# Kernel tuning notes

Hardware: AMD Instinct MI355X
Metric: run time of the kernel (lower is better)

## Reference

```python
import jax, jax.numpy as jnp
import numpy as np

WINDOW_SIZE = 11
SIGMA = 1.5
C1 = 0.01 ** 2
C2 = 0.03 ** 2


def _make_window(window_size, channel):
    x = np.arange(window_size) - window_size // 2
    g = np.exp(-(x ** 2) / (2.0 * SIGMA ** 2))
    g = g / g.sum()
    w2d = np.outer(g, g).astype(np.float32)  # [K,K]
    # depthwise kernel [C, 1, K, K]
    return jnp.asarray(np.broadcast_to(w2d, (channel, 1, window_size, window_size)).copy())


def _dw_conv(x, window, channel):
    pad = WINDOW_SIZE // 2
    return jax.lax.conv_general_dilated(
        x, window, window_strides=(1, 1), padding=[(pad, pad), (pad, pad)],
        dimension_numbers=('NCHW', 'OIHW', 'NCHW'), feature_group_count=channel)


def setup_inputs() -> dict:
    key = jax.random.key(0)
    k1, k2 = jax.random.split(key)
    shape = (16, 3, 512, 512)
    img1 = jax.random.uniform(k1, shape, dtype=jnp.float32)
    img2 = jax.random.uniform(k2, shape, dtype=jnp.float32)
    return {"img1": img1, "img2": img2}


def reference(img1, img2):
    channel = img1.shape[1]
    window = _make_window(WINDOW_SIZE, channel).astype(img1.dtype)

    mu1 = _dw_conv(img1, window, channel)
    mu2 = _dw_conv(img2, window, channel)
    mu1_sq = mu1 * mu1
    mu2_sq = mu2 * mu2
    mu1_mu2 = mu1 * mu2

    sigma1_sq = _dw_conv(img1 * img1, window, channel) - mu1_sq
    sigma2_sq = _dw_conv(img2 * img2, window, channel) - mu2_sq
    sigma12 = _dw_conv(img1 * img2, window, channel) - mu1_mu2

    ssim_map = ((2 * mu1_mu2 + C1) * (2 * sigma12 + C2)) / (
        (mu1_sq + mu2_sq + C1) * (sigma1_sq + sigma2_sq + C2))
    return jnp.mean(ssim_map)  # size_average=True
```

## Files before the change

kernel.cpp:

```cpp
#include <hip/hip_runtime.h>
#include <math.h>

#define IMG_H 512
#define IMG_W 512
#define TH 8
#define KR 5
#define KS 11
#define NR (TH + 2 * KR)
#define LWE 524
#define NTHREADS 512
#define NBANDS (IMG_H / TH)
#define NPLANES 48
#define NBLK (NBANDS * NPLANES)

typedef float f32x2 __attribute__((ext_vector_type(2)));
typedef float f32x4 __attribute__((ext_vector_type(4)));

struct W22 { float w[2 * KS]; };

__device__ __forceinline__ int swz(int e) { return e ^ ((e >> 3) & 7); }

__global__ __launch_bounds__(NTHREADS, 4)
void ssim_tile_kernel(const float* __restrict__ img1, const float* __restrict__ img2,
                      float* __restrict__ bsums, W22 wt) {
    __shared__ f32x4 sE[TH][LWE];
    __shared__ float redw[NTHREADS / 64];

    const int bid   = blockIdx.x;
    const int sbid  = (bid & 7) * (NBLK / 8) + (bid >> 3);
    const int plane = sbid >> 6;
    const int band  = sbid & (NBANDS - 1);

    const int r0 = band * TH - KR;
    const float* __restrict__ p1 = img1 + (size_t)plane * (IMG_H * IMG_W);
    const float* __restrict__ p2 = img2 + (size_t)plane * (IMG_H * IMG_W);
    const int tid = threadIdx.x;

    if (tid < 128) {
        const int h = tid & 15;
        if (h < 12) {
            const int r = tid >> 4;
            const int e = (h < 6) ? h : (512 + h);
            sE[r][swz(e)] = (f32x4){0.f, 0.f, 0.f, 0.f};
        }
    }

    float av[NR], bv[NR];
    {
        const float* __restrict__ g1 = p1 + tid;
        const float* __restrict__ g2 = p2 + tid;
        if (r0 >= 0 && r0 + NR <= IMG_H) {
            #pragma unroll
            for (int j = 0; j < NR; ++j) {
                av[j] = g1[(r0 + j) * IMG_W];
                bv[j] = g2[(r0 + j) * IMG_W];
            }
        } else {
            #pragma unroll
            for (int j = 0; j < NR; ++j) {
                const int  rr  = r0 + j;
                const bool ok  = (rr >= 0) && (rr < IMG_H);
                const int  rrc = min(max(rr, 0), IMG_H - 1);
                const float a = g1[rrc * IMG_W];
                const float b = g2[rrc * IMG_W];
                av[j] = ok ? a : 0.f;
                bv[j] = ok ? b : 0.f;
            }
        }
    }

    f32x4 acc[TH];
    #pragma unroll
    for (int r = 0; r < TH; ++r) acc[r] = (f32x4){0.f, 0.f, 0.f, 0.f};

    #pragma unroll
    for (int j = 0; j < NR; ++j) {
        const float a = av[j], b = bv[j];
        f32x4 pv; pv.x = a; pv.y = b;
        pv.z = fmaf(a, a, b * b); pv.w = a * b;
        #pragma unroll
        for (int r = 0; r < TH; ++r) {
            const int k = j - r;
            if (k >= 0 && k < KS) {
                f32x4 wv; wv.x = wt.w[2*k]; wv.y = wt.w[2*k + 1];
                wv.z = wt.w[2*k]; wv.w = wt.w[2*k + 1];
                acc[r] = __builtin_elementwise_fma(wv, pv, acc[r]);
            }
        }
    }
    {
        const int slot = swz(tid + 6);
        #pragma unroll
        for (int r = 0; r < TH; ++r) sE[r][slot] = acc[r];
    }
    __syncthreads();

    const float C1f = 0.0001f;
    const float C2f = 0.0009f;
    const int g  = tid >> 6;
    const int L  = tid & 63;
    const int eb = (L << 3) + 1;

    f32x4 x[18];
    #pragma unroll
    for (int i = 0; i < 18; ++i) x[i] = sE[g][swz(eb + i)];

    float lsum = 0.f;
    #pragma unroll
    for (int jj = 0; jj < 8; ++jj) {
        f32x4 c;
        {
            f32x4 wv; wv.x = wt.w[0]; wv.y = wt.w[1];
            wv.z = wt.w[0]; wv.w = wt.w[1];
            c = wv * x[jj];
        }
        #pragma unroll
        for (int k = 1; k < KS; ++k) {
            f32x4 wv; wv.x = wt.w[2*k]; wv.y = wt.w[2*k + 1];
            wv.z = wt.w[2*k]; wv.w = wt.w[2*k + 1];
            c = __builtin_elementwise_fma(wv, x[jj + k], c);
        }
        const float m1 = c.x, m2 = c.y;
        const float pp = c.z, ab = c.w;
        const float mu11 = m1 * m1;
        const float mu22 = m2 * m2;
        const float mu12 = m1 * m2;
        const float t     = mu11 + mu22;
        const float sigpp = pp - t;
        const float sig12 = ab - mu12;
        const float num = fmaf(2.f, mu12, C1f) * fmaf(2.f, sig12, C2f);
        const float den = (t + C1f) * (sigpp + C2f);
        lsum = fmaf(num, __builtin_amdgcn_rcpf(den), lsum);
    }

    #pragma unroll
    for (int off = 32; off > 0; off >>= 1) lsum += __shfl_down(lsum, off);
    if ((tid & 63) == 0) redw[tid >> 6] = lsum;
    __syncthreads();
    if (tid == 0) {
        float t = 0.f;
        #pragma unroll
        for (int w = 0; w < NTHREADS / 64; ++w) t += redw[w];
        bsums[sbid] = t;
    }
}

__global__ __launch_bounds__(256)
void ssim_reduce_kernel(const float4* __restrict__ bsums, int n4,
                        float* __restrict__ out, double inv_count) {
    __shared__ double red[256];
    double acc = 0.0;
    for (int i = threadIdx.x; i < n4; i += 256) {
        const float4 v = bsums[i];
        acc += (double)v.x + (double)v.y + (double)v.z + (double)v.w;
    }
    red[threadIdx.x] = acc;
    __syncthreads();
    #pragma unroll
    for (int off = 128; off > 0; off >>= 1) {
        if (threadIdx.x < off) red[threadIdx.x] += red[threadIdx.x + off];
        __syncthreads();
    }
    if (threadIdx.x == 0) out[0] = (float)(red[0] * inv_count);
}

extern "C" void kernel_launch(void* const* d_in, const int* in_sizes, int n_in,
                              void* d_out, int out_size, void* d_ws, size_t ws_size,
                              hipStream_t stream) {
    const float* img1 = (const float*)d_in[0];
    const float* img2 = (const float*)d_in[1];
    float* out = (float*)d_out;
    float* bsums = (float*)d_ws;

    W22 wt;
    {
        double g[KS], sum = 0.0;
        for (int i = 0; i < KS; ++i) {
            const double x = (double)(i - KR);
            g[i] = exp(-(x * x) / (2.0 * 1.5 * 1.5));
            sum += g[i];
        }
        for (int i = 0; i < KS; ++i) {
            wt.w[2*i]     = (float)(g[i] / sum);
            wt.w[2*i + 1] = (float)(g[i] / sum);
        }
    }

    ssim_tile_kernel<<<dim3(NBLK), NTHREADS, 0, stream>>>(img1, img2, bsums, wt);

    const double inv_count = 1.0 / ((double)NPLANES * IMG_H * IMG_W);
    ssim_reduce_kernel<<<1, 256, 0, stream>>>((const float4*)bsums, NBLK / 4,
                                              out, inv_count);
}
```

Baseline: 40.69 us.

## Stage input rows into LDS via direct global_load_lds instead of register loads

Each block now DMA-copies its 18 halo rows of both images straight into shared memory with 16-byte global_load_lds, replacing the 36 scalar per-thread register loads. The vertical pass then reads from LDS, and the same buffer is reused for the horizontal-pass tile after an extra barrier. The aim is fewer load instructions, wider transactions and lower VGPR pressure, so memory latency is handled better. In exchange the LDS footprint grows slightly, an extra synchronisation and an LDS round trip are added, and edge rows are clamped and then zeroed at read time.

```diff
diff --git a/kernel.cpp b/kernel.cpp
--- a/kernel.cpp
+++ b/kernel.cpp
@@ -13,7 +13,10 @@
 #define NPLANES 48
 #define NBLK (NBANDS * NPLANES)
 
-typedef float f32x2 __attribute__((ext_vector_type(2)));
+#define ROWB (IMG_W * 4)
+#define RAWBYTES (NR * 2 * ROWB)
+#define NCHUNK (RAWBYTES / 1024)
+
 typedef float f32x4 __attribute__((ext_vector_type(4)));
 
 struct W22 { float w[2 * KS]; };
@@ -23,7 +26,7 @@
 __global__ __launch_bounds__(NTHREADS, 4)
 void ssim_tile_kernel(const float* __restrict__ img1, const float* __restrict__ img2,
                       float* __restrict__ bsums, W22 wt) {
-    __shared__ f32x4 sE[TH][LWE];
+    __shared__ __align__(16) char lds[RAWBYTES];
     __shared__ float redw[NTHREADS / 64];
 
     const int bid   = blockIdx.x;
@@ -34,40 +37,28 @@
     const int r0 = band * TH - KR;
     const float* __restrict__ p1 = img1 + (size_t)plane * (IMG_H * IMG_W);
     const float* __restrict__ p2 = img2 + (size_t)plane * (IMG_H * IMG_W);
-    const int tid = threadIdx.x;
+    const int tid  = threadIdx.x;
+    const int lane = tid & 63;
+    const int wid  = tid >> 6;
 
-    if (tid < 128) {
-        const int h = tid & 15;
-        if (h < 12) {
-            const int r = tid >> 4;
-            const int e = (h < 6) ? h : (512 + h);
-            sE[r][swz(e)] = (f32x4){0.f, 0.f, 0.f, 0.f};
-        }
+    #pragma unroll
+    for (int i = 0; i < NCHUNK / 8; ++i) {
+        const int c    = wid * (NCHUNK / 8) + i;
+        const int isb  = (c >= NCHUNK / 2);
+        const int cc   = isb ? c - NCHUNK / 2 : c;
+        const int rr   = cc >> 1;
+        const int half = cc & 1;
+        const int rrc  = min(max(r0 + rr, 0), IMG_H - 1);
+        const float* gsrc = (isb ? p2 : p1) + rrc * IMG_W + half * 256 + lane * 4;
+        __builtin_amdgcn_global_load_lds(
+            (const __attribute__((address_space(1))) unsigned int*)gsrc,
+            (__attribute__((address_space(3))) unsigned int*)(lds + c * 1024),
+            16, 0, 0);
     }
+    __syncthreads();
 
-    float av[NR], bv[NR];
-    {
-        const float* __restrict__ g1 = p1 + tid;
-        const float* __restrict__ g2 = p2 + tid;
-        if (r0 >= 0 && r0 + NR <= IMG_H) {
-            #pragma unroll
-            for (int j = 0; j < NR; ++j) {
-                av[j] = g1[(r0 + j) * IMG_W];
-                bv[j] = g2[(r0 + j) * IMG_W];
-            }
-        } else {
-            #pragma unroll
-            for (int j = 0; j < NR; ++j) {
-                const int  rr  = r0 + j;
-                const bool ok  = (rr >= 0) && (rr < IMG_H);
-                const int  rrc = min(max(rr, 0), IMG_H - 1);
-                const float a = g1[rrc * IMG_W];
-                const float b = g2[rrc * IMG_W];
-                av[j] = ok ? a : 0.f;
-                bv[j] = ok ? b : 0.f;
-            }
-        }
-    }
+    const float* __restrict__ sa = (const float*)lds;
+    const float* __restrict__ sb = (const float*)(lds + NR * ROWB);
 
     f32x4 acc[TH];
     #pragma unroll
@@ -75,7 +66,11 @@
 
     #pragma unroll
     for (int j = 0; j < NR; ++j) {
-        const float a = av[j], b = bv[j];
+        const int  rr = r0 + j;
+        const bool ok = (rr >= 0) && (rr < IMG_H);
+        float a = sa[j * IMG_W + tid];
+        float b = sb[j * IMG_W + tid];
+        if (!ok) { a = 0.f; b = 0.f; }
         f32x4 pv; pv.x = a; pv.y = b;
         pv.z = fmaf(a, a, b * b); pv.w = a * b;
         #pragma unroll
@@ -88,6 +83,17 @@
             }
         }
     }
+    __syncthreads();
+
+    f32x4 (* __restrict__ sE)[LWE] = (f32x4 (*)[LWE])lds;
+    if (tid < 128) {
+        const int h = tid & 15;
+        if (h < 12) {
+            const int r = tid >> 4;
+            const int e = (h < 6) ? h : (512 + h);
+            sE[r][swz(e)] = (f32x4){0.f, 0.f, 0.f, 0.f};
+        }
+    }
     {
         const int slot = swz(tid + 6);
         #pragma unroll
@@ -97,9 +103,8 @@
 
     const float C1f = 0.0001f;
     const float C2f = 0.0009f;
-    const int g  = tid >> 6;
-    const int L  = tid & 63;
-    const int eb = (L << 3) + 1;
+    const int g  = wid;
+    const int eb = (lane << 3) + 1;
 
     f32x4 x[18];
     #pragma unroll
@@ -135,7 +140,7 @@
 
     #pragma unroll
     for (int off = 32; off > 0; off >>= 1) lsum += __shfl_down(lsum, off);
-    if ((tid & 63) == 0) redw[tid >> 6] = lsum;
+    if (lane == 0) redw[wid] = lsum;
     __syncthreads();
     if (tid == 0) {
         float t = 0.f;
```

Result: slower. 51.30 us (+26.1%).
